# Kernel tuning notes

Measured on AMD Instinct MI355X. Metric: run time of the kernel, lower is better.

The kernel has to match this reference:

```python
import jax, jax.numpy as jnp
import numpy as np

N = 50000          # num nodes
E = 800000         # num edges
IN_C, HID_C, OUT_C = 128, 256, 256
LN_EPS = 1e-5


def gcn_conv(x, W, b, row, col):
    """PyG GCNConv: h = D^{-1/2}(A+I)D^{-1/2} (x W) + b, self-loops added."""
    h = x @ W                                             # [N, C_out]
    deg = jax.ops.segment_sum(jnp.ones((row.shape[0],), h.dtype), col,
                              num_segments=N) + 1.0        # +1 for self-loop
    dinv = jax.lax.rsqrt(deg)                              # [N]
    msg = h[row] * (dinv[row] * dinv[col])[:, None]        # [E, C_out] gathered msgs
    agg = jax.ops.segment_sum(msg, col, num_segments=N)
    agg = agg + h * (dinv * dinv)[:, None]                 # self-loop contribution
    return agg + b


def layer_norm(x, gamma, beta):
    mu = jnp.mean(x, axis=-1, keepdims=True)
    var = jnp.mean(jnp.square(x - mu), axis=-1, keepdims=True)
    return (x - mu) * jax.lax.rsqrt(var + LN_EPS) * gamma + beta


def setup_inputs() -> dict:
    key = jax.random.key(0)
    ks = jax.random.split(key, 8)
    x = jax.random.normal(ks[0], (N, IN_C), jnp.float32)
    edge_index = jax.random.randint(ks[1], (2, E), 0, N, dtype=jnp.int64)
    W1 = jax.random.normal(ks[2], (IN_C, HID_C), jnp.float32) * (1.0 / np.sqrt(IN_C))
    b1 = jnp.zeros((HID_C,), jnp.float32)
    W2 = jax.random.normal(ks[3], (HID_C, OUT_C), jnp.float32) * (1.0 / np.sqrt(HID_C))
    b2 = jnp.zeros((OUT_C,), jnp.float32)
    ln1_g = jnp.ones((HID_C,), jnp.float32); ln1_b = jnp.zeros((HID_C,), jnp.float32)
    ln2_g = jnp.ones((OUT_C,), jnp.float32); ln2_b = jnp.zeros((OUT_C,), jnp.float32)
    proj_W = jax.random.normal(ks[4], (IN_C, OUT_C), jnp.float32) * (1.0 / np.sqrt(IN_C))
    proj_b = jnp.zeros((OUT_C,), jnp.float32)
    return {"x": x, "edge_index": edge_index, "W1": W1, "b1": b1, "W2": W2,
            "b2": b2, "ln1_g": ln1_g, "ln1_b": ln1_b, "ln2_g": ln2_g,
            "ln2_b": ln2_b, "proj_W": proj_W, "proj_b": proj_b}


def reference(x, edge_index, W1, b1, W2, b2, ln1_g, ln1_b, ln2_g, ln2_b,
              proj_W, proj_b):
    row, col = edge_index[0], edge_index[1]   # messages flow row -> col
    identity = x @ proj_W + proj_b            # self.proj (Linear, in != out)
    h = gcn_conv(x, W1, b1, row, col)
    h = jax.nn.relu(layer_norm(h, ln1_g, ln1_b))   # dropout = identity (eval)
    g = gcn_conv(h, W2, b2, row, col)
    g = layer_norm(g, ln2_g, ln2_b)
    return jax.nn.relu(g + identity)
```

## Files before the change

kernel.cpp:

```cpp
#include <hip/hip_runtime.h>

#define NN 50000
#define NE 800000
#define LN_EPS 1e-5f

using bf16x8 = __attribute__((ext_vector_type(8))) short;
using f32x4  = __attribute__((ext_vector_type(4))) float;

__device__ __forceinline__ float b2f(unsigned short u) {
    union { unsigned int i; float f; } c;
    c.i = ((unsigned int)u) << 16;
    return c.f;
}
__device__ __forceinline__ unsigned short f2b(float f) {
    union { float f; unsigned int i; } c;
    c.f = f;
    const unsigned int i = c.i;
    return (unsigned short)((i + 0x7FFFu + ((i >> 16) & 1u)) >> 16);
}

template <int ITERS>
__device__ __forceinline__ void stage_async(const short* __restrict__ g,
                                            short* __restrict__ l) {
    const int lane = threadIdx.x & 63;
    const int wv = threadIdx.x >> 6;
#pragma unroll
    for (int i = 0; i < ITERS; ++i) {
        const int u = i * 256 + wv * 64;
        __builtin_amdgcn_global_load_lds(
            (const __attribute__((address_space(1))) void*)(g + (size_t)(u + lane) * 8),
            (__attribute__((address_space(3))) void*)(l + (size_t)u * 8),
            16, 0, 0);
    }
}

__global__ __launch_bounds__(256) void cvt_k(const float* __restrict__ X,
                                             short* __restrict__ Xb, int n4) {
    const int i = blockIdx.x * 256 + threadIdx.x;
    if (i >= n4) return;
    const float4 v = ((const float4*)X)[i];
    ushort4 o;
    o.x = f2b(v.x); o.y = f2b(v.y); o.z = f2b(v.z); o.w = f2b(v.w);
    ((ushort4*)Xb)[i] = o;
}

template <int K>
__global__ __launch_bounds__(256) void pack_w_k(const float* __restrict__ W,
                                                short* __restrict__ Wp) {
    constexpr int KB = K / 32;
    const int i = blockIdx.x * 256 + threadIdx.x;
    const int j = i & 7;
    const int l = (i >> 3) & 63;
    const int t = i >> 9;
    const int kb = t % KB;
    const int nt = t / KB;
    const int k = 32 * kb + 8 * (l >> 4) + j;
    const int n = 16 * nt + (l & 15);
    Wp[i] = (short)f2b(W[(size_t)k * 256 + n]);
}

__global__ __launch_bounds__(256) void count_k(const int* __restrict__ col,
                                               int* __restrict__ rowptr) {
    const int e = blockIdx.x * 256 + threadIdx.x;
    if (e < NE) atomicAdd(&rowptr[col[e] + 1], 1);
}

__global__ __launch_bounds__(256) void block_sum_k(const int* __restrict__ p,
                                                   int* __restrict__ psum, int n) {
    __shared__ int sh[256];
    const int t = threadIdx.x;
    const int i = blockIdx.x * 256 + t;
    sh[t] = (i < n) ? p[i] : 0;
    __syncthreads();
#pragma unroll
    for (int off = 128; off > 0; off >>= 1) {
        if (t < off) sh[t] += sh[t + off];
        __syncthreads();
    }
    if (t == 0) psum[blockIdx.x] = sh[0];
}

__global__ __launch_bounds__(256) void scan_apply_k(int* __restrict__ p,
                                                    const int* __restrict__ psum,
                                                    int n, int nblk) {
    __shared__ int sh[256];
    const int t = threadIdx.x;
    const int b = blockIdx.x;
    const int i = b * 256 + t;
    sh[t] = (t < b && t < nblk) ? psum[t] : 0;
    __syncthreads();
#pragma unroll
    for (int off = 128; off > 0; off >>= 1) {
        if (t < off) sh[t] += sh[t + off];
        __syncthreads();
    }
    const int carry = sh[0];
    __syncthreads();
    sh[t] = (i < n) ? p[i] : 0;
    __syncthreads();
#pragma unroll
    for (int off = 1; off < 256; off <<= 1) {
        const int u = (t >= off) ? sh[t - off] : 0;
        __syncthreads();
        sh[t] += u;
        __syncthreads();
    }
    if (i < n) p[i] = sh[t] + carry;
}

__global__ __launch_bounds__(256) void dinv_k(const int* __restrict__ rowptr,
                                              float* __restrict__ dinv) {
    const int i = blockIdx.x * 256 + threadIdx.x;
    if (i < NN) dinv[i] = rsqrtf((float)(rowptr[i + 1] - rowptr[i]) + 1.0f);
}

__global__ __launch_bounds__(256) void fill_k(const int* __restrict__ row,
                                              const int* __restrict__ col,
                                              const float* __restrict__ dinv,
                                              int* __restrict__ rowptr,
                                              int* __restrict__ srcs,
                                              float* __restrict__ wvals) {
    const int e = blockIdx.x * 256 + threadIdx.x;
    if (e >= NE) return;
    const int rr = row[e];
    const int pos = atomicAdd(&rowptr[col[e]], 1);
    srcs[pos] = rr;
    wvals[pos] = dinv[rr];
}

__global__ __launch_bounds__(256) void gather1_k(const short* __restrict__ X,
                                                 const int* __restrict__ endptr,
                                                 const int* __restrict__ srcs,
                                                 const float* __restrict__ wvals,
                                                 const float* __restrict__ dinv,
                                                 short* __restrict__ A1) {
    const int node = blockIdx.x * 4 + (threadIdx.x >> 6);
    const int lane = threadIdx.x & 63;
    if (node >= NN) return;
    const int start = node ? endptr[node - 1] : 0;
    const int end = endptr[node];

    float a0 = 0.f, a1 = 0.f;
    int j = start;
    for (; j + 3 < end; j += 4) {
        const int s0 = srcs[j], s1 = srcs[j + 1], s2 = srcs[j + 2], s3 = srcs[j + 3];
        const float w0 = wvals[j], w1 = wvals[j + 1];
        const float w2 = wvals[j + 2], w3 = wvals[j + 3];
        const ushort2 v0 = ((const ushort2*)(X + (size_t)s0 * 128))[lane];
        const ushort2 v1 = ((const ushort2*)(X + (size_t)s1 * 128))[lane];
        const ushort2 v2 = ((const ushort2*)(X + (size_t)s2 * 128))[lane];
        const ushort2 v3 = ((const ushort2*)(X + (size_t)s3 * 128))[lane];
        a0 += b2f(v0.x) * w0 + b2f(v1.x) * w1 + b2f(v2.x) * w2 + b2f(v3.x) * w3;
        a1 += b2f(v0.y) * w0 + b2f(v1.y) * w1 + b2f(v2.y) * w2 + b2f(v3.y) * w3;
    }
    for (; j < end; ++j) {
        const int s0 = srcs[j];
        const float w0 = wvals[j];
        const ushort2 v0 = ((const ushort2*)(X + (size_t)s0 * 128))[lane];
        a0 += b2f(v0.x) * w0;
        a1 += b2f(v0.y) * w0;
    }
    const float dc = dinv[node];
    const ushort2 h = ((const ushort2*)(X + (size_t)node * 128))[lane];
    a0 = (a0 + b2f(h.x) * dc) * dc;
    a1 = (a1 + b2f(h.y) * dc) * dc;
    ushort2 o;
    o.x = f2b(a0); o.y = f2b(a1);
    ((ushort2*)A1)[(size_t)node * 64 + lane] = o;
}

__global__ __launch_bounds__(256) void gather2_k(const short* __restrict__ H,
                                                 const int* __restrict__ endptr,
                                                 const int* __restrict__ srcs,
                                                 const float* __restrict__ wvals,
                                                 const float* __restrict__ dinv,
                                                 short* __restrict__ agg) {
    const int node = blockIdx.x * 4 + (threadIdx.x >> 6);
    const int lane = threadIdx.x & 63;
    if (node >= NN) return;
    const int start = node ? endptr[node - 1] : 0;
    const int end = endptr[node];

    float a0 = 0.f, a1 = 0.f, a2 = 0.f, a3 = 0.f;
    int j = start;
    for (; j + 3 < end; j += 4) {
        const int s0 = srcs[j], s1 = srcs[j + 1], s2 = srcs[j + 2], s3 = srcs[j + 3];
        const float w0 = wvals[j], w1 = wvals[j + 1];
        const float w2 = wvals[j + 2], w3 = wvals[j + 3];
        const ushort4 v0 = ((const ushort4*)(H + (size_t)s0 * 256))[lane];
        const ushort4 v1 = ((const ushort4*)(H + (size_t)s1 * 256))[lane];
        const ushort4 v2 = ((const ushort4*)(H + (size_t)s2 * 256))[lane];
        const ushort4 v3 = ((const ushort4*)(H + (size_t)s3 * 256))[lane];
        a0 += b2f(v0.x) * w0 + b2f(v1.x) * w1 + b2f(v2.x) * w2 + b2f(v3.x) * w3;
        a1 += b2f(v0.y) * w0 + b2f(v1.y) * w1 + b2f(v2.y) * w2 + b2f(v3.y) * w3;
        a2 += b2f(v0.z) * w0 + b2f(v1.z) * w1 + b2f(v2.z) * w2 + b2f(v3.z) * w3;
        a3 += b2f(v0.w) * w0 + b2f(v1.w) * w1 + b2f(v2.w) * w2 + b2f(v3.w) * w3;
    }
    for (; j < end; ++j) {
        const int s0 = srcs[j];
        const float w0 = wvals[j];
        const ushort4 v0 = ((const ushort4*)(H + (size_t)s0 * 256))[lane];
        a0 += b2f(v0.x) * w0;
        a1 += b2f(v0.y) * w0;
        a2 += b2f(v0.z) * w0;
        a3 += b2f(v0.w) * w0;
    }
    const float dc = dinv[node];
    const ushort4 h = ((const ushort4*)(H + (size_t)node * 256))[lane];
    ushort4 o;
    o.x = f2b((a0 + b2f(h.x) * dc) * dc);
    o.y = f2b((a1 + b2f(h.y) * dc) * dc);
    o.z = f2b((a2 + b2f(h.z) * dc) * dc);
    o.w = f2b((a3 + b2f(h.w) * dc) * dc);
    ((ushort4*)agg)[(size_t)node * 64 + lane] = o;
}

template <int K, bool PROJ, bool OUT_BF16>
__global__ __launch_bounds__(256) void gemm_ln_k(
    const short* __restrict__ X, const short* __restrict__ Wp,
    const float* __restrict__ bias, const float* __restrict__ gamma,
    const float* __restrict__ beta, const short* __restrict__ Xp,
    const short* __restrict__ Wpp, const float* __restrict__ pbias,
    void* __restrict__ Yv) {
    constexpr int KB = K / 32;
    constexpr int CHUNK = 2048 * KB;
    __shared__ short lds[2][CHUNK];
    const int lane = threadIdx.x & 63;
    const int wv = threadIdx.x >> 6;
    const int row0 = blockIdx.x * 64 + wv * 16;
    const int r = row0 + (lane & 15);
    const int rc = (r < NN) ? r : (NN - 1);
    const int kof = 8 * (lane >> 4);
    const int colbase = lane & 15;

    bf16x8 a[KB];
#pragma unroll
    for (int kb = 0; kb < KB; ++kb)
        a[kb] = *(const bf16x8*)(X + (size_t)rc * K + 32 * kb + kof);
    bf16x8 ap[4];
    if (PROJ) {
#pragma unroll
        for (int kb = 0; kb < 4; ++kb)
            ap[kb] = *(const bf16x8*)(Xp + (size_t)rc * 128 + 32 * kb + kof);
    }

    stage_async<KB>(Wp, lds[0]);

    f32x4 acc[16];
#pragma unroll
    for (int c = 0; c < 4; ++c) {
        __syncthreads();
        if (c < 3)
            stage_async<KB>(Wp + (size_t)(c + 1) * CHUNK, lds[(c + 1) & 1]);
        else if (PROJ)
            stage_async<4>(Wpp, lds[0]);
        const short* buf = lds[c & 1];
#pragma unroll
        for (int ntl = 0; ntl < 4; ++ntl) {
            f32x4 cacc = {0.f, 0.f, 0.f, 0.f};
#pragma unroll
            for (int kb = 0; kb < KB; ++kb) {
                const bf16x8 b = ((const bf16x8*)buf)[(ntl * KB + kb) * 64 + lane];
                cacc = __builtin_amdgcn_mfma_f32_16x16x32_bf16(a[kb], b, cacc, 0, 0, 0);
            }
            acc[c * 4 + ntl] = cacc;
        }
    }

    float s[4] = {0.f, 0.f, 0.f, 0.f};
    float q[4] = {0.f, 0.f, 0.f, 0.f};
#pragma unroll
    for (int nt = 0; nt < 16; ++nt) {
        const float bv = bias[nt * 16 + colbase];
#pragma unroll
        for (int rg = 0; rg < 4; ++rg) {
            const float v = acc[nt][rg] + bv;
            acc[nt][rg] = v;
            s[rg] += v;
            q[rg] += v * v;
        }
    }
#pragma unroll
    for (int off = 1; off < 16; off <<= 1) {
#pragma unroll
        for (int rg = 0; rg < 4; ++rg) {
            s[rg] += __shfl_xor(s[rg], off, 64);
            q[rg] += __shfl_xor(q[rg], off, 64);
        }
    }
    float mu[4], rsd[4];
#pragma unroll
    for (int rg = 0; rg < 4; ++rg) {
        mu[rg] = s[rg] * (1.f / 256.f);
        const float var = q[rg] * (1.f / 256.f) - mu[rg] * mu[rg];
        rsd[rg] = rsqrtf(var + LN_EPS);
    }

    const int orow0 = row0 + (lane >> 4) * 4;
    if (PROJ) {
#pragma unroll
        for (int pc = 0; pc < 4; ++pc) {
            __syncthreads();
            if (pc < 3)
                stage_async<4>(Wpp + (size_t)(pc + 1) * 8192, lds[(pc + 1) & 1]);
            const short* buf = lds[pc & 1];
#pragma unroll
            for (int ntl = 0; ntl < 4; ++ntl) {
                const int nt = pc * 4 + ntl;
                f32x4 pid = {0.f, 0.f, 0.f, 0.f};
#pragma unroll
                for (int kb = 0; kb < 4; ++kb) {
                    const bf16x8 b = ((const bf16x8*)buf)[(ntl * 4 + kb) * 64 + lane];
                    pid = __builtin_amdgcn_mfma_f32_16x16x32_bf16(ap[kb], b, pid, 0, 0, 0);
                }
                const int col = nt * 16 + colbase;
                const float g = gamma[col];
                const float be = beta[col];
                const float pbv = pbias[col];
#pragma unroll
                for (int rg = 0; rg < 4; ++rg) {
                    const int orow = orow0 + rg;
                    float v = (acc[nt][rg] - mu[rg]) * rsd[rg] * g + be;
                    v += pid[rg] + pbv;
                    v = fmaxf(v, 0.f);
                    if (orow < NN) {
                        if (OUT_BF16)
                            ((short*)Yv)[(size_t)orow * 256 + col] = (short)f2b(v);
                        else
                            ((float*)Yv)[(size_t)orow * 256 + col] = v;
                    }
                }
            }
        }
    } else {
#pragma unroll
        for (int nt = 0; nt < 16; ++nt) {
            const int col = nt * 16 + colbase;
            const float g = gamma[col];
            const float be = beta[col];
#pragma unroll
            for (int rg = 0; rg < 4; ++rg) {
                const int orow = orow0 + rg;
                float v = (acc[nt][rg] - mu[rg]) * rsd[rg] * g + be;
                v = fmaxf(v, 0.f);
                if (orow < NN) {
                    if (OUT_BF16)
                        ((short*)Yv)[(size_t)orow * 256 + col] = (short)f2b(v);
                    else
                        ((float*)Yv)[(size_t)orow * 256 + col] = v;
                }
            }
        }
    }
}

extern "C" void kernel_launch(void* const* d_in, const int* in_sizes, int n_in,
                              void* d_out, int out_size, void* d_ws, size_t ws_size,
                              hipStream_t stream) {
    const float* x    = (const float*)d_in[0];
    const int*   eidx = (const int*)d_in[1];
    const float* W1   = (const float*)d_in[2];
    const float* b1   = (const float*)d_in[3];
    const float* W2   = (const float*)d_in[4];
    const float* b2   = (const float*)d_in[5];
    const float* ln1g = (const float*)d_in[6];
    const float* ln1b = (const float*)d_in[7];
    const float* ln2g = (const float*)d_in[8];
    const float* ln2b = (const float*)d_in[9];
    const float* pW   = (const float*)d_in[10];
    const float* pb   = (const float*)d_in[11];

    const int* row = eidx;
    const int* col = eidx + NE;
    float* out = (float*)d_out;

    short* xb     = (short*)d_ws;
    short* A1     = xb + (size_t)NN * 128;
    short* Bb     = A1 + (size_t)NN * 128;
    short* Ag     = Bb + (size_t)NN * 256;
    float* dinv   = (float*)(Ag + (size_t)NN * 256);
    int*   rowptr = (int*)(dinv + NN);
    int*   psum   = rowptr + NN + 4;
    int*   srcs   = psum + 256;
    float* wvals  = (float*)(srcs + NE);
    short* Wp1    = (short*)(wvals + NE);
    short* Wp2    = Wp1 + 128 * 256;
    short* Wpp    = Wp2 + 256 * 256;

    const int nscan = NN + 1;
    const int nblk = (nscan + 255) / 256;

    cvt_k<<<(NN * 128 / 4 + 255) / 256, 256, 0, stream>>>(x, xb, NN * 128 / 4);
    pack_w_k<128><<<128, 256, 0, stream>>>(W1, Wp1);
    pack_w_k<256><<<256, 256, 0, stream>>>(W2, Wp2);
    pack_w_k<128><<<128, 256, 0, stream>>>(pW, Wpp);

    hipMemsetAsync(rowptr, 0, (NN + 4) * sizeof(int), stream);
    count_k<<<(NE + 255) / 256, 256, 0, stream>>>(col, rowptr);
    block_sum_k<<<nblk, 256, 0, stream>>>(rowptr, psum, nscan);
    scan_apply_k<<<nblk, 256, 0, stream>>>(rowptr, psum, nscan, nblk);
    dinv_k<<<(NN + 255) / 256, 256, 0, stream>>>(rowptr, dinv);
    fill_k<<<(NE + 255) / 256, 256, 0, stream>>>(row, col, dinv, rowptr, srcs, wvals);

    gather1_k<<<(NN + 3) / 4, 256, 0, stream>>>(xb, rowptr, srcs, wvals, dinv, A1);
    gemm_ln_k<128, false, true><<<(NN + 63) / 64, 256, 0, stream>>>(
        A1, Wp1, b1, ln1g, ln1b, nullptr, nullptr, nullptr, Bb);

    gather2_k<<<(NN + 3) / 4, 256, 0, stream>>>(Bb, rowptr, srcs, wvals, dinv, Ag);
    gemm_ln_k<256, true, false><<<(NN + 63) / 64, 256, 0, stream>>>(
        Ag, Wp2, b2, ln2g, ln2b, xb, Wpp, pb, out);
}
```

Before: 286.8 us.

## Merge prep kernels, pack CSR pairs, and use persistent full-LDS-weight GEMMs

Folds the x conversion and the three weight-pack kernels into one launch, and computes dinv inside the scan kernel. Source indices and weights are stored as interleaved int2 pairs so each edge needs one load. The GEMMs become persistent 512-thread kernels with 256 blocks that stage the whole packed weight set into 128 KB of dynamic LDS once, instead of double-buffering chunks per tile. The projection GEMM moves into the first GEMM and writes fp32 identity to the output buffer, which the second GEMM reads back and updates in place. This adds an extra fp32 read and write of the output and may lower occupancy because of the large LDS footprint.

Result: slower. 492.9 us (+71.9%).

```diff
diff --git a/kernel.cpp b/kernel.cpp
--- a/kernel.cpp
+++ b/kernel.cpp
@@ -3,6 +3,8 @@
 #define NN 50000
 #define NE 800000
 #define LN_EPS 1e-5f
+#define NGROUP 391
+#define GRID_GEMM 256
 
 using bf16x8 = __attribute__((ext_vector_type(8))) short;
 using f32x4  = __attribute__((ext_vector_type(4))) float;
@@ -19,14 +21,14 @@
     return (unsigned short)((i + 0x7FFFu + ((i >> 16) & 1u)) >> 16);
 }
 
-template <int ITERS>
-__device__ __forceinline__ void stage_async(const short* __restrict__ g,
-                                            short* __restrict__ l) {
+template <int UNITS>
+__device__ __forceinline__ void stage512(const short* __restrict__ g,
+                                         short* __restrict__ l) {
     const int lane = threadIdx.x & 63;
     const int wv = threadIdx.x >> 6;
 #pragma unroll
-    for (int i = 0; i < ITERS; ++i) {
-        const int u = i * 256 + wv * 64;
+    for (int i = 0; i < UNITS / 512; ++i) {
+        const int u = i * 512 + wv * 64;
         __builtin_amdgcn_global_load_lds(
             (const __attribute__((address_space(1))) void*)(g + (size_t)(u + lane) * 8),
             (__attribute__((address_space(3))) void*)(l + (size_t)u * 8),
@@ -34,21 +36,10 @@
     }
 }
 
-__global__ __launch_bounds__(256) void cvt_k(const float* __restrict__ X,
-                                             short* __restrict__ Xb, int n4) {
-    const int i = blockIdx.x * 256 + threadIdx.x;
-    if (i >= n4) return;
-    const float4 v = ((const float4*)X)[i];
-    ushort4 o;
-    o.x = f2b(v.x); o.y = f2b(v.y); o.z = f2b(v.z); o.w = f2b(v.w);
-    ((ushort4*)Xb)[i] = o;
-}
-
 template <int K>
-__global__ __launch_bounds__(256) void pack_w_k(const float* __restrict__ W,
-                                                short* __restrict__ Wp) {
+__device__ __forceinline__ void pack_body(const float* __restrict__ W,
+                                          short* __restrict__ Wp, int i) {
     constexpr int KB = K / 32;
-    const int i = blockIdx.x * 256 + threadIdx.x;
     const int j = i & 7;
     const int l = (i >> 3) & 63;
     const int t = i >> 9;
@@ -59,6 +50,27 @@
     Wp[i] = (short)f2b(W[(size_t)k * 256 + n]);
 }
 
+__global__ __launch_bounds__(256) void prep_k(
+    const float* __restrict__ x, const float* __restrict__ W1,
+    const float* __restrict__ W2, const float* __restrict__ pW,
+    short* __restrict__ xb, short* __restrict__ Wp1,
+    short* __restrict__ Wp2, short* __restrict__ Wpp) {
+    const int b = blockIdx.x;
+    if (b < 6250) {
+        const int i = b * 256 + threadIdx.x;
+        const float4 v = ((const float4*)x)[i];
+        ushort4 o;
+        o.x = f2b(v.x); o.y = f2b(v.y); o.z = f2b(v.z); o.w = f2b(v.w);
+        ((ushort4*)xb)[i] = o;
+    } else if (b < 6250 + 128) {
+        pack_body<128>(W1, Wp1, (b - 6250) * 256 + threadIdx.x);
+    } else if (b < 6250 + 384) {
+        pack_body<256>(W2, Wp2, (b - 6378) * 256 + threadIdx.x);
+    } else {
+        pack_body<128>(pW, Wpp, (b - 6634) * 256 + threadIdx.x);
+    }
+}
+
 __global__ __launch_bounds__(256) void count_k(const int* __restrict__ col,
                                                int* __restrict__ rowptr) {
     const int e = blockIdx.x * 256 + threadIdx.x;
@@ -82,6 +94,7 @@
 
 __global__ __launch_bounds__(256) void scan_apply_k(int* __restrict__ p,
                                                     const int* __restrict__ psum,
+                                                    float* __restrict__ dinv,
                                                     int n, int nblk) {
     __shared__ int sh[256];
     const int t = threadIdx.x;
@@ -96,7 +109,9 @@
     }
     const int carry = sh[0];
     __syncthreads();
-    sh[t] = (i < n) ? p[i] : 0;
+    const int raw = (i < n) ? p[i] : 0;
+    if (i >= 1 && i < n) dinv[i - 1] = rsqrtf((float)raw + 1.0f);
+    sh[t] = raw;
     __syncthreads();
 #pragma unroll
     for (int off = 1; off < 256; off <<= 1) {
@@ -108,30 +123,24 @@
     if (i < n) p[i] = sh[t] + carry;
 }
 
-__global__ __launch_bounds__(256) void dinv_k(const int* __restrict__ rowptr,
-                                              float* __restrict__ dinv) {
-    const int i = blockIdx.x * 256 + threadIdx.x;
-    if (i < NN) dinv[i] = rsqrtf((float)(rowptr[i + 1] - rowptr[i]) + 1.0f);
-}
-
 __global__ __launch_bounds__(256) void fill_k(const int* __restrict__ row,
                                               const int* __restrict__ col,
                                               const float* __restrict__ dinv,
                                               int* __restrict__ rowptr,
-                                              int* __restrict__ srcs,
-                                              float* __restrict__ wvals) {
+                                              int2* __restrict__ pairs) {
     const int e = blockIdx.x * 256 + threadIdx.x;
     if (e >= NE) return;
     const int rr = row[e];
     const int pos = atomicAdd(&rowptr[col[e]], 1);
-    srcs[pos] = rr;
-    wvals[pos] = dinv[rr];
+    int2 pr;
+    pr.x = rr;
+    pr.y = __float_as_int(dinv[rr]);
+    pairs[pos] = pr;
 }
 
 __global__ __launch_bounds__(256) void gather1_k(const short* __restrict__ X,
                                                  const int* __restrict__ endptr,
-                                                 const int* __restrict__ srcs,
-                                                 const float* __restrict__ wvals,
+                                                 const int2* __restrict__ pairs,
                                                  const float* __restrict__ dinv,
                                                  short* __restrict__ A1) {
     const int node = blockIdx.x * 4 + (threadIdx.x >> 6);
@@ -143,20 +152,21 @@
     float a0 = 0.f, a1 = 0.f;
     int j = start;
     for (; j + 3 < end; j += 4) {
-        const int s0 = srcs[j], s1 = srcs[j + 1], s2 = srcs[j + 2], s3 = srcs[j + 3];
-        const float w0 = wvals[j], w1 = wvals[j + 1];
-        const float w2 = wvals[j + 2], w3 = wvals[j + 3];
-        const ushort2 v0 = ((const ushort2*)(X + (size_t)s0 * 128))[lane];
-        const ushort2 v1 = ((const ushort2*)(X + (size_t)s1 * 128))[lane];
-        const ushort2 v2 = ((const ushort2*)(X + (size_t)s2 * 128))[lane];
-        const ushort2 v3 = ((const ushort2*)(X + (size_t)s3 * 128))[lane];
+        const int2 p0 = pairs[j], p1 = pairs[j + 1];
+        const int2 p2 = pairs[j + 2], p3 = pairs[j + 3];
+        const float w0 = __int_as_float(p0.y), w1 = __int_as_float(p1.y);
+        const float w2 = __int_as_float(p2.y), w3 = __int_as_float(p3.y);
+        const ushort2 v0 = ((const ushort2*)(X + (size_t)p0.x * 128))[lane];
+        const ushort2 v1 = ((const ushort2*)(X + (size_t)p1.x * 128))[lane];
+        const ushort2 v2 = ((const ushort2*)(X + (size_t)p2.x * 128))[lane];
+        const ushort2 v3 = ((const ushort2*)(X + (size_t)p3.x * 128))[lane];
         a0 += b2f(v0.x) * w0 + b2f(v1.x) * w1 + b2f(v2.x) * w2 + b2f(v3.x) * w3;
         a1 += b2f(v0.y) * w0 + b2f(v1.y) * w1 + b2f(v2.y) * w2 + b2f(v3.y) * w3;
     }
     for (; j < end; ++j) {
-        const int s0 = srcs[j];
-        const float w0 = wvals[j];
-        const ushort2 v0 = ((const ushort2*)(X + (size_t)s0 * 128))[lane];
+        const int2 p0 = pairs[j];
+        const float w0 = __int_as_float(p0.y);
+        const ushort2 v0 = ((const ushort2*)(X + (size_t)p0.x * 128))[lane];
         a0 += b2f(v0.x) * w0;
         a1 += b2f(v0.y) * w0;
     }
@@ -171,8 +181,7 @@
 
 __global__ __launch_bounds__(256) void gather2_k(const short* __restrict__ H,
                                                  const int* __restrict__ endptr,
-                                                 const int* __restrict__ srcs,
-                                                 const float* __restrict__ wvals,
+                                                 const int2* __restrict__ pairs,
                                                  const float* __restrict__ dinv,
                                                  short* __restrict__ agg) {
     const int node = blockIdx.x * 4 + (threadIdx.x >> 6);
@@ -184,22 +193,23 @@
     float a0 = 0.f, a1 = 0.f, a2 = 0.f, a3 = 0.f;
     int j = start;
     for (; j + 3 < end; j += 4) {
-        const int s0 = srcs[j], s1 = srcs[j + 1], s2 = srcs[j + 2], s3 = srcs[j + 3];
-        const float w0 = wvals[j], w1 = wvals[j + 1];
-        const float w2 = wvals[j + 2], w3 = wvals[j + 3];
-        const ushort4 v0 = ((const ushort4*)(H + (size_t)s0 * 256))[lane];
-        const ushort4 v1 = ((const ushort4*)(H + (size_t)s1 * 256))[lane];
-        const ushort4 v2 = ((const ushort4*)(H + (size_t)s2 * 256))[lane];
-        const ushort4 v3 = ((const ushort4*)(H + (size_t)s3 * 256))[lane];
+        const int2 p0 = pairs[j], p1 = pairs[j + 1];
+        const int2 p2 = pairs[j + 2], p3 = pairs[j + 3];
+        const float w0 = __int_as_float(p0.y), w1 = __int_as_float(p1.y);
+        const float w2 = __int_as_float(p2.y), w3 = __int_as_float(p3.y);
+        const ushort4 v0 = ((const ushort4*)(H + (size_t)p0.x * 256))[lane];
+        const ushort4 v1 = ((const ushort4*)(H + (size_t)p1.x * 256))[lane];
+        const ushort4 v2 = ((const ushort4*)(H + (size_t)p2.x * 256))[lane];
+        const ushort4 v3 = ((const ushort4*)(H + (size_t)p3.x * 256))[lane];
         a0 += b2f(v0.x) * w0 + b2f(v1.x) * w1 + b2f(v2.x) * w2 + b2f(v3.x) * w3;
         a1 += b2f(v0.y) * w0 + b2f(v1.y) * w1 + b2f(v2.y) * w2 + b2f(v3.y) * w3;
         a2 += b2f(v0.z) * w0 + b2f(v1.z) * w1 + b2f(v2.z) * w2 + b2f(v3.z) * w3;
         a3 += b2f(v0.w) * w0 + b2f(v1.w) * w1 + b2f(v2.w) * w2 + b2f(v3.w) * w3;
     }
     for (; j < end; ++j) {
-        const int s0 = srcs[j];
-        const float w0 = wvals[j];
-        const ushort4 v0 = ((const ushort4*)(H + (size_t)s0 * 256))[lane];
+        const int2 p0 = pairs[j];
+        const float w0 = __int_as_float(p0.y);
+        const ushort4 v0 = ((const ushort4*)(H + (size_t)p0.x * 256))[lane];
         a0 += b2f(v0.x) * w0;
         a1 += b2f(v0.y) * w0;
         a2 += b2f(v0.z) * w0;
@@ -215,139 +225,185 @@
     ((ushort4*)agg)[(size_t)node * 64 + lane] = o;
 }
 
-template <int K, bool PROJ, bool OUT_BF16>
-__global__ __launch_bounds__(256) void gemm_ln_k(
-    const short* __restrict__ X, const short* __restrict__ Wp,
-    const float* __restrict__ bias, const float* __restrict__ gamma,
-    const float* __restrict__ beta, const short* __restrict__ Xp,
-    const short* __restrict__ Wpp, const float* __restrict__ pbias,
-    void* __restrict__ Yv) {
-    constexpr int KB = K / 32;
-    constexpr int CHUNK = 2048 * KB;
-    __shared__ short lds[2][CHUNK];
+__global__ __launch_bounds__(512) void gemm1_k(
+    const short* __restrict__ A1, const short* __restrict__ xb,
+    const short* __restrict__ Wboth, const float* __restrict__ bias,
+    const float* __restrict__ gamma, const float* __restrict__ beta,
+    const float* __restrict__ pbias, short* __restrict__ Bb,
+    float* __restrict__ ident) {
+    extern __shared__ short lds[];
+    stage512<8192>(Wboth, lds);
     const int lane = threadIdx.x & 63;
     const int wv = threadIdx.x >> 6;
-    const int row0 = blockIdx.x * 64 + wv * 16;
-    const int r = row0 + (lane & 15);
-    const int rc = (r < NN) ? r : (NN - 1);
     const int kof = 8 * (lane >> 4);
     const int colbase = lane & 15;
-
-    bf16x8 a[KB];
-#pragma unroll
-    for (int kb = 0; kb < KB; ++kb)
-        a[kb] = *(const bf16x8*)(X + (size_t)rc * K + 32 * kb + kof);
-    bf16x8 ap[4];
-    if (PROJ) {
-#pragma unroll
-        for (int kb = 0; kb < 4; ++kb)
-            ap[kb] = *(const bf16x8*)(Xp + (size_t)rc * 128 + 32 * kb + kof);
-    }
-
-    stage_async<KB>(Wp, lds[0]);
-
-    f32x4 acc[16];
-#pragma unroll
-    for (int c = 0; c < 4; ++c) {
-        __syncthreads();
-        if (c < 3)
-            stage_async<KB>(Wp + (size_t)(c + 1) * CHUNK, lds[(c + 1) & 1]);
-        else if (PROJ)
-            stage_async<4>(Wpp, lds[0]);
-        const short* buf = lds[c & 1];
-#pragma unroll
-        for (int ntl = 0; ntl < 4; ++ntl) {
-            f32x4 cacc = {0.f, 0.f, 0.f, 0.f};
-#pragma unroll
-            for (int kb = 0; kb < KB; ++kb) {
-                const bf16x8 b = ((const bf16x8*)buf)[(ntl * KB + kb) * 64 + lane];
-                cacc = __builtin_amdgcn_mfma_f32_16x16x32_bf16(a[kb], b, cacc, 0, 0, 0);
-            }
-            acc[c * 4 + ntl] = cacc;
-        }
-    }
-
-    float s[4] = {0.f, 0.f, 0.f, 0.f};
-    float q[4] = {0.f, 0.f, 0.f, 0.f};
-#pragma unroll
-    for (int nt = 0; nt < 16; ++nt) {
-        const float bv = bias[nt * 16 + colbase];
+    const short* W1l = lds;
+    const short* Wpl = lds + 32768;
+    __syncthreads();
+
+    for (int g = blockIdx.x; g < NGROUP; g += GRID_GEMM) {
+        const int row0 = g * 128 + wv * 16;
+        const int r = row0 + (lane & 15);
+        const int rc = (r < NN) ? r : (NN - 1);
+        bf16x8 a[4], ap[4];
+#pragma unroll
+        for (int kb = 0; kb < 4; ++kb) {
+            a[kb] = *(const bf16x8*)(A1 + (size_t)rc * 128 + 32 * kb + kof);
+            ap[kb] = *(const bf16x8*)(xb + (size_t)rc * 128 + 32 * kb + kof);
+        }
+
+        f32x4 acc[16];
+#pragma unroll
+        for (int nt = 0; nt < 16; ++nt) {
+            f32x4 c = {0.f, 0.f, 0.f, 0.f};
+#pragma unroll
+            for (int kb = 0; kb < 4; ++kb) {
+                const bf16x8 b = ((const bf16x8*)W1l)[(nt * 4 + kb) * 64 + lane];
+                c = __builtin_amdgcn_mfma_f32_16x16x32_bf16(a[kb], b, c, 0, 0, 0);
+            }
+            acc[nt] = c;
+        }
+
+        float s[4] = {0.f, 0.f, 0.f, 0.f};
+        float q[4] = {0.f, 0.f, 0.f, 0.f};
+#pragma unroll
+        for (int nt = 0; nt < 16; ++nt) {
+            const float bv = bias[nt * 16 + colbase];
+#pragma unroll
+            for (int rg = 0; rg < 4; ++rg) {
+                const float v = acc[nt][rg] + bv;
+                acc[nt][rg] = v;
+                s[rg] += v;
+                q[rg] += v * v;
+            }
+        }
+#pragma unroll
+        for (int off = 1; off < 16; off <<= 1) {
+#pragma unroll
+            for (int rg = 0; rg < 4; ++rg) {
+                s[rg] += __shfl_xor(s[rg], off, 64);
+                q[rg] += __shfl_xor(q[rg], off, 64);
+            }
+        }
+        float mu[4], rsd[4];
 #pragma unroll
         for (int rg = 0; rg < 4; ++rg) {
-            const float v = acc[nt][rg] + bv;
-            acc[nt][rg] = v;
-            s[rg] += v;
-            q[rg] += v * v;
-        }
-    }
-#pragma unroll
-    for (int off = 1; off < 16; off <<= 1) {
+            mu[rg] = s[rg] * (1.f / 256.f);
+            const float var = q[rg] * (1.f / 256.f) - mu[rg] * mu[rg];
+            rsd[rg] = rsqrtf(var + LN_EPS);
+        }
+
+        const int orow0 = row0 + (lane >> 4) * 4;
+#pragma unroll
+        for (int nt = 0; nt < 16; ++nt) {
+            const int col = nt * 16 + colbase;
+            const float gm = gamma[col];
+            const float be = beta[col];
+#pragma unroll
+            for (int rg = 0; rg < 4; ++rg) {
+                const int orow = orow0 + rg;
+                float v = (acc[nt][rg] - mu[rg]) * rsd[rg] * gm + be;
+                v = fmaxf(v, 0.f);
+                if (orow < NN)
+                    Bb[(size_t)orow * 256 + col] = (short)f2b(v);
+            }
+        }
+
+#pragma unroll
+        for (int nt = 0; nt < 16; ++nt) {
+            f32x4 pid = {0.f, 0.f, 0.f, 0.f};
+#pragma unroll
+            for (int kb = 0; kb < 4; ++kb) {
+                const bf16x8 b = ((const bf16x8*)Wpl)[(nt * 4 + kb) * 64 + lane];
+                pid = __builtin_amdgcn_mfma_f32_16x16x32_bf16(ap[kb], b, pid, 0, 0, 0);
+            }
+            const int col = nt * 16 + colbase;
+            const float pbv = pbias[col];
+#pragma unroll
+            for (int rg = 0; rg < 4; ++rg) {
+                const int orow = orow0 + rg;
+                if (orow < NN)
+                    ident[(size_t)orow * 256 + col] = pid[rg] + pbv;
+            }
+        }
+    }
+}
+
+__global__ __launch_bounds__(512) void gemm2_k(
+    const short* __restrict__ Ag, const short* __restrict__ Wp2,
+    const float* __restrict__ bias, const float* __restrict__ gamma,
+    const float* __restrict__ beta, float* io) {
+    extern __shared__ short lds[];
+    stage512<8192>(Wp2, lds);
+    const int lane = threadIdx.x & 63;
+    const int wv = threadIdx.x >> 6;
+    const int kof = 8 * (lane >> 4);
+    const int colbase = lane & 15;
+    __syncthreads();
+
+    for (int g = blockIdx.x; g < NGROUP; g += GRID_GEMM) {
+        const int row0 = g * 128 + wv * 16;
+        const int r = row0 + (lane & 15);
+        const int rc = (r < NN) ? r : (NN - 1);
+        bf16x8 a[8];
+#pragma unroll
+        for (int kb = 0; kb < 8; ++kb)
+            a[kb] = *(const bf16x8*)(Ag + (size_t)rc * 256 + 32 * kb + kof);
+
+        f32x4 acc[16];
+#pragma unroll
+        for (int nt = 0; nt < 16; ++nt) {
+            f32x4 c = {0.f, 0.f, 0.f, 0.f};
+#pragma unroll
+            for (int kb = 0; kb < 8; ++kb) {
+                const bf16x8 b = ((const bf16x8*)lds)[(nt * 8 + kb) * 64 + lane];
+                c = __builtin_amdgcn_mfma_f32_16x16x32_bf16(a[kb], b, c, 0, 0, 0);
+            }
+            acc[nt] = c;
+        }
+
+        float s[4] = {0.f, 0.f, 0.f, 0.f};
+        float q[4] = {0.f, 0.f, 0.f, 0.f};
+#pragma unroll
+        for (int nt = 0; nt < 16; ++nt) {
+            const float bv = bias[nt * 16 + colbase];
+#pragma unroll
+            for (int rg = 0; rg < 4; ++rg) {
+                const float v = acc[nt][rg] + bv;
+                acc[nt][rg] = v;
+                s[rg] += v;
+                q[rg] += v * v;
+            }
+        }
+#pragma unroll
+        for (int off = 1; off < 16; off <<= 1) {
+#pragma unroll
+            for (int rg = 0; rg < 4; ++rg) {
+                s[rg] += __shfl_xor(s[rg], off, 64);
+                q[rg] += __shfl_xor(q[rg], off, 64);
+            }
+        }
+        float mu[4], rsd[4];
 #pragma unroll
         for (int rg = 0; rg < 4; ++rg) {
-            s[rg] += __shfl_xor(s[rg], off, 64);
-            q[rg] += __shfl_xor(q[rg], off, 64);
-        }
-    }
-    float mu[4], rsd[4];
-#pragma unroll
-    for (int rg = 0; rg < 4; ++rg) {
-        mu[rg] = s[rg] * (1.f / 256.f);
-        const float var = q[rg] * (1.f / 256.f) - mu[rg] * mu[rg];
-        rsd[rg] = rsqrtf(var + LN_EPS);
-    }
-
-    const int orow0 = row0 + (lane >> 4) * 4;
-    if (PROJ) {
-#pragma unroll
-        for (int pc = 0; pc < 4; ++pc) {
-            __syncthreads();
-            if (pc < 3)
-                stage_async<4>(Wpp + (size_t)(pc + 1) * 8192, lds[(pc + 1) & 1]);
-            const short* buf = lds[pc & 1];
-#pragma unroll
-            for (int ntl = 0; ntl < 4; ++ntl) {
-                const int nt = pc * 4 + ntl;
-                f32x4 pid = {0.f, 0.f, 0.f, 0.f};
-#pragma unroll
-                for (int kb = 0; kb < 4; ++kb) {
-                    const bf16x8 b = ((const bf16x8*)buf)[(ntl * 4 + kb) * 64 + lane];
-                    pid = __builtin_amdgcn_mfma_f32_16x16x32_bf16(ap[kb], b, pid, 0, 0, 0);
-                }
-                const int col = nt * 16 + colbase;
-                const float g = gamma[col];
-                const float be = beta[col];
-                const float pbv = pbias[col];
-#pragma unroll
-                for (int rg = 0; rg < 4; ++rg) {
-                    const int orow = orow0 + rg;
-                    float v = (acc[nt][rg] - mu[rg]) * rsd[rg] * g + be;
-                    v += pid[rg] + pbv;
-                    v = fmaxf(v, 0.f);
-                    if (orow < NN) {
-                        if (OUT_BF16)
-                            ((short*)Yv)[(size_t)orow * 256 + col] = (short)f2b(v);
-                        else
-                            ((float*)Yv)[(size_t)orow * 256 + col] = v;
-                    }
-                }
-            }
-        }
-    } else {
+            mu[rg] = s[rg] * (1.f / 256.f);
+            const float var = q[rg] * (1.f / 256.f) - mu[rg] * mu[rg];
+            rsd[rg] = rsqrtf(var + LN_EPS);
+        }
+
+        const int orow0 = row0 + (lane >> 4) * 4;
 #pragma unroll
         for (int nt = 0; nt < 16; ++nt) {
             const int col = nt * 16 + colbase;
-            const float g = gamma[col];
+            const float gm = gamma[col];
             const float be = beta[col];
 #pragma unroll
             for (int rg = 0; rg < 4; ++rg) {
                 const int orow = orow0 + rg;
-                float v = (acc[nt][rg] - mu[rg]) * rsd[rg] * g + be;
-                v = fmaxf(v, 0.f);
                 if (orow < NN) {
-                    if (OUT_BF16)
-                        ((short*)Yv)[(size_t)orow * 256 + col] = (short)f2b(v);
-                    else
-                        ((float*)Yv)[(size_t)orow * 256 + col] = v;
+                    float v = (acc[nt][rg] - mu[rg]) * rsd[rg] * gm + be;
+                    v += io[(size_t)orow * 256 + col];
+                    io[(size_t)orow * 256 + col] = fmaxf(v, 0.f);
                 }
             }
         }
@@ -381,32 +437,30 @@
     float* dinv   = (float*)(Ag + (size_t)NN * 256);
     int*   rowptr = (int*)(dinv + NN);
     int*   psum   = rowptr + NN + 4;
-    int*   srcs   = psum + 256;
-    float* wvals  = (float*)(srcs + NE);
-    short* Wp1    = (short*)(wvals + NE);
-    short* Wp2    = Wp1 + 128 * 256;
-    short* Wpp    = Wp2 + 256 * 256;
+    int2*  pairs  = (int2*)(psum + 256);
+    short* Wp1    = (short*)(pairs + NE);
+    short* Wpp    = Wp1 + 128 * 256;
+    short* Wp2    = Wpp + 128 * 256;
 
     const int nscan = NN + 1;
     const int nblk = (nscan + 255) / 256;
 
-    cvt_k<<<(NN * 128 / 4 + 255) / 256, 256, 0, stream>>>(x, xb, NN * 128 / 4);
-    pack_w_k<128><<<128, 256, 0, stream>>>(W1, Wp1);
-    pack_w_k<256><<<256, 256, 0, stream>>>(W2, Wp2);
-    pack_w_k<128><<<128, 256, 0, stream>>>(pW, Wpp);
+    hipFuncSetAttribute((const void*)gemm1_k,
+                        hipFuncAttributeMaxDynamicSharedMemorySize, 131072);
+    hipFuncSetAttribute((const void*)gemm2_k,
+                        hipFuncAttributeMaxDynamicSharedMemorySize, 131072);
 
     hipMemsetAsync(rowptr, 0, (NN + 4) * sizeof(int), stream);
+    prep_k<<<6762, 256, 0, stream>>>(x, W1, W2, pW, xb, Wp1, Wp2, Wpp);
     count_k<<<(NE + 255) / 256, 256, 0, stream>>>(col, rowptr);
     block_sum_k<<<nblk, 256, 0, stream>>>(rowptr, psum, nscan);
-    scan_apply_k<<<nblk, 256, 0, stream>>>(rowptr, psum, nscan, nblk);
-    dinv_k<<<(NN + 255) / 256, 256, 0, stream>>>(rowptr, dinv);
-    fill_k<<<(NE + 255) / 256, 256, 0, stream>>>(row, col, dinv, rowptr, srcs, wvals);
-
-    gather1_k<<<(NN + 3) / 4, 256, 0, stream>>>(xb, rowptr, srcs, wvals, dinv, A1);
-    gemm_ln_k<128, false, true><<<(NN + 63) / 64, 256, 0, stream>>>(
-        A1, Wp1, b1, ln1g, ln1b, nullptr, nullptr, nullptr, Bb);
-
-    gather2_k<<<(NN + 3) / 4, 256, 0, stream>>>(Bb, rowptr, srcs, wvals, dinv, Ag);
-    gemm_ln_k<256, true, false><<<(NN + 63) / 64, 256, 0, stream>>>(
-        Ag, Wp2, b2, ln2g, ln2b, xb, Wpp, pb, out);
-}
+    scan_apply_k<<<nblk, 256, 0, stream>>>(rowptr, psum, dinv, nscan, nblk);
+    fill_k<<<(NE + 255) / 256, 256, 0, stream>>>(row, col, dinv, rowptr, pairs);
+
+    gather1_k<<<(NN + 3) / 4, 256, 0, stream>>>(xb, rowptr, pairs, dinv, A1);
+    gemm1_k<<<GRID_GEMM, 512, 131072, stream>>>(A1, xb, Wp1, b1, ln1g, ln1b,
+                                                pb, Bb, out);
+
+    gather2_k<<<(NN + 3) / 4, 256, 0, stream>>>(Bb, rowptr, pairs, dinv, Ag);
+    gemm2_k<<<GRID_GEMM, 512, 131072, stream>>>(Ag, Wp2, b2, ln2g, ln2b, out);
+}
```
